# Performance work log

Measured on AMD Instinct MI355X. Metric: run time of the kernel, lower is better.

## Reference

```python
import jax, jax.numpy as jnp
import numpy as np

B, S, H = 2, 2048, 2048
FFN = 1024
E = 8
TOP_K = 2


def setup_inputs() -> dict:
    key = jax.random.key(0)
    ks = jax.random.split(key, 5)
    scale = 0.02
    hidden_states = jax.random.normal(ks[0], (B, S, H), dtype=jnp.float32)
    Wg = jax.random.normal(ks[1], (E, H), dtype=jnp.float32) * scale   # gate: Linear(H, E) weight
    W1 = jax.random.normal(ks[2], (E, FFN, H), dtype=jnp.float32) * scale  # stacked w1 per expert
    W3 = jax.random.normal(ks[3], (E, FFN, H), dtype=jnp.float32) * scale  # stacked w3 per expert
    W2 = jax.random.normal(ks[4], (E, H, FFN), dtype=jnp.float32) * scale  # stacked w2 per expert
    bias = jnp.zeros((E,), dtype=jnp.float32)  # e_score_correction_bias buffer
    return {"hidden_states": hidden_states, "Wg": Wg, "W1": W1, "W2": W2, "W3": W3, "bias": bias}


def reference(hidden_states, Wg, W1, W2, W3, bias):
    bsz, seq_len, hidden_dim = hidden_states.shape
    x = hidden_states.reshape(-1, hidden_dim)                 # [T, H]
    router_logits = x @ Wg.T                                  # [T, E]
    routing_weights = jax.nn.sigmoid(router_logits.astype(jnp.float32))
    scores = routing_weights + bias                           # bias only affects selection
    _, top_k_index = jax.lax.top_k(scores, TOP_K)             # [T, K]
    top_k_weights = jnp.take_along_axis(routing_weights, top_k_index, axis=1)
    top_k_weights = top_k_weights / top_k_weights.sum(axis=-1, keepdims=True)
    top_k_weights = top_k_weights.astype(x.dtype)
    # per-token per-expert combine weight (0 for non-selected experts)
    one_hot = jax.nn.one_hot(top_k_index, Wg.shape[0], dtype=x.dtype)  # [T, K, E]
    expert_w = jnp.einsum('tk,tke->te', top_k_weights, one_hot)        # [T, E]
    # SwiGLU expert MLPs applied via stacked (grouped) GEMMs
    h1 = jnp.einsum('th,efh->tef', x, W1)                     # [T, E, FFN]
    h3 = jnp.einsum('th,efh->tef', x, W3)
    g = jax.nn.silu(h1) * h3 * expert_w[:, :, None]           # scale before down-proj
    out = jnp.einsum('tef,ehf->th', g, W2)                    # weighted combine
    return out.reshape(bsz, seq_len, hidden_dim)
```

## Files before the change

kernel.cpp:

```cpp
#include <hip/hip_runtime.h>
#include <hip/hip_bf16.h>


#define T_TOK 4096
#define H_DIM 2048
#define FFN_D 1024
#define NE    8

typedef __attribute__((ext_vector_type(8))) short          bf16x8;
typedef __attribute__((ext_vector_type(4))) float          f32x4;
typedef __attribute__((ext_vector_type(4))) unsigned short us4;

__device__ __forceinline__ unsigned short f2bf(float f) {
  unsigned u = __builtin_bit_cast(unsigned, f);
  u += 0x7fffu + ((u >> 16) & 1u);
  return (unsigned short)(u >> 16);
}
__device__ __forceinline__ float bf2f(unsigned short u) {
  return __builtin_bit_cast(float, ((unsigned)u) << 16);
}
__device__ __forceinline__ void async16(const void* g, void* l) {
  __builtin_amdgcn_global_load_lds((const __attribute__((address_space(1))) void*)g,
                                   (__attribute__((address_space(3))) void*)l, 16, 0, 0);
}

__global__ void router2_kernel(const float* __restrict__ x,
                               const float* __restrict__ Wg,
                               const float* __restrict__ bias,
                               unsigned* __restrict__ epair,
                               float* __restrict__ wpair,
                               unsigned short* __restrict__ Xb) {
  const int wv   = threadIdx.x >> 6;
  const int lane = threadIdx.x & 63;
  const int t    = blockIdx.x * 4 + wv;

  const float4* xr = (const float4*)(x + (size_t)t * H_DIM);
  us4*          xb = (us4*)(Xb + (size_t)t * H_DIM);

  float acc[NE];
#pragma unroll
  for (int e = 0; e < NE; e++) acc[e] = 0.f;

#pragma unroll
  for (int j = 0; j < 8; j++) {
    int i4 = j * 64 + lane;
    float4 v = xr[i4];
    us4 d; d.x = f2bf(v.x); d.y = f2bf(v.y); d.z = f2bf(v.z); d.w = f2bf(v.w);
    xb[i4] = d;
#pragma unroll
    for (int e = 0; e < NE; e++) {
      float4 w = ((const float4*)(Wg + e * H_DIM))[i4];
      acc[e] += v.x * w.x + v.y * w.y + v.z * w.z + v.w * w.w;
    }
  }
#pragma unroll
  for (int e = 0; e < NE; e++) {
#pragma unroll
    for (int m = 32; m >= 1; m >>= 1) acc[e] += __shfl_xor(acc[e], m, 64);
  }

  if (lane == 0) {
    float sig[NE], sc[NE];
#pragma unroll
    for (int e = 0; e < NE; e++) {
      sig[e] = 1.f / (1.f + expf(-acc[e]));
      sc[e]  = sig[e] + bias[e];
    }
    int i1 = 0; float v1 = sc[0];
#pragma unroll
    for (int e = 1; e < NE; e++) if (sc[e] > v1) { v1 = sc[e]; i1 = e; }
    int i2 = -1; float v2 = -1e30f;
#pragma unroll
    for (int e = 0; e < NE; e++) if (e != i1 && sc[e] > v2) { v2 = sc[e]; i2 = e; }
    float w1 = sig[i1], w2 = sig[i2];
    float s = w1 + w2;
    epair[t] = (unsigned)i1 | ((unsigned)i2 << 8);
    wpair[2 * t]     = w1 / s;
    wpair[2 * t + 1] = w2 / s;
  }
}

__global__ void compact_kernel(const unsigned* __restrict__ epair,
                               const float* __restrict__ wpair,
                               int* __restrict__ cnt,
                               int* __restrict__ base,
                               int* __restrict__ rows,
                               float* __restrict__ wts,
                               int* __restrict__ t2s) {
  const int e    = threadIdx.x >> 6;
  const int lane = threadIdx.x & 63;
  const unsigned long long ltmask = ((unsigned long long)1 << lane) - 1;
  __shared__ int cnts[NE];

  int count = 0;
  for (int c = 0; c < T_TOK; c += 64) {
    int t = c + lane;
    unsigned ep = epair[t];
    bool m1 = ((ep & 255u) == (unsigned)e);
    bool m2 = (((ep >> 8) & 255u) == (unsigned)e);
    unsigned long long b1 = __ballot(m1);
    if (m1) {
      int p = count + __popcll(b1 & ltmask);
      rows[e * T_TOK + p] = t;
      wts [e * T_TOK + p] = wpair[2 * t];
      t2s[2 * t] = (e << 12) | p;
    }
    count += __popcll(b1);
    unsigned long long b2 = __ballot(m2);
    if (m2) {
      int p = count + __popcll(b2 & ltmask);
      rows[e * T_TOK + p] = t;
      wts [e * T_TOK + p] = wpair[2 * t + 1];
      t2s[2 * t + 1] = (e << 12) | p;
    }
    count += __popcll(b2);
  }
  if (lane == 0) { cnts[e] = count; cnt[e] = count; }
  __syncthreads();
  if (threadIdx.x == 0) {
    int s = 0;
    for (int i = 0; i < NE; i++) { base[i] = s; s += cnts[i]; }
    base[NE] = s;
  }
}

__global__ void convert2_kernel(const float* __restrict__ a, unsigned short* __restrict__ da,
                                const float* __restrict__ b, unsigned short* __restrict__ db) {
  const size_t N4 = (size_t)NE * FFN_D * H_DIM / 4;
  size_t i = (size_t)blockIdx.x * 256 + threadIdx.x;
  const float* s; unsigned short* d;
  if (i < N4) { s = a; d = da; } else { s = b; d = db; i -= N4; }
  float4 v = ((const float4*)s)[i];
  us4 o; o.x = f2bf(v.x); o.y = f2bf(v.y); o.z = f2bf(v.z); o.w = f2bf(v.w);
  ((us4*)d)[i] = o;
}
__global__ void convert_kernel(const float* __restrict__ s, unsigned short* __restrict__ d) {
  size_t i = (size_t)blockIdx.x * 256 + threadIdx.x;
  float4 v = ((const float4*)s)[i];
  us4 o; o.x = f2bf(v.x); o.y = f2bf(v.y); o.z = f2bf(v.z); o.w = f2bf(v.w);
  ((us4*)d)[i] = o;
}

__launch_bounds__(256)
__global__ void upproj_fast(const unsigned short* __restrict__ Xb,
                            const unsigned short* __restrict__ W1b,
                            const unsigned short* __restrict__ W3b,
                            const int* __restrict__ cnt,
                            const int* __restrict__ base,
                            const int* __restrict__ rows,
                            const float* __restrict__ wts,
                            unsigned short* __restrict__ G) {
  const int e  = blockIdx.z;
  const int m0 = blockIdx.y * 128;
  const int n0 = blockIdx.x * 64;
  const int ce = cnt[e];
  if (m0 >= ce) return;

  __shared__ __align__(16) unsigned short As [2 * 128 * 32];
  __shared__ __align__(16) unsigned short B1s[2 * 64 * 32];
  __shared__ __align__(16) unsigned short B3s[2 * 64 * 32];
  __shared__ int   t_ids[128];
  __shared__ float w_lds[128];

  const int tid = threadIdx.x;
  if (tid < 128) {
    int i = m0 + tid;
    if (i < ce) { t_ids[tid] = rows[e * T_TOK + i]; w_lds[tid] = wts[e * T_TOK + i]; }
    else        { t_ids[tid] = 0;                   w_lds[tid] = 0.f; }
  }
  __syncthreads();

  const int lane = tid & 63;
  const int wv   = tid >> 6;

  const unsigned short* gA[2];
#pragma unroll
  for (int c = 0; c < 2; c++) {
    int r = wv * 32 + c * 16 + (lane >> 2);
    gA[c] = Xb + (size_t)t_ids[r] * H_DIM + (lane & 3) * 8;
  }
  const size_t wrow = (size_t)(n0 + wv * 16 + (lane >> 2));
  const unsigned short* gB1 = W1b + (size_t)e * FFN_D * H_DIM + wrow * H_DIM + (lane & 3) * 8;
  const unsigned short* gB3 = W3b + (size_t)e * FFN_D * H_DIM + wrow * H_DIM + (lane & 3) * 8;

  const int wm = (wv & 1) * 64;
  const int wn = (wv >> 1) * 32;
  const int qk = (lane >> 4) * 8;
  const int lr = lane & 15;

  f32x4 acc1[4][2], acc3[4][2];
#pragma unroll
  for (int mi = 0; mi < 4; mi++)
#pragma unroll
    for (int ni = 0; ni < 2; ni++) { acc1[mi][ni] = (f32x4)0.f; acc3[mi][ni] = (f32x4)0.f; }

  for (int kt = 0; kt < H_DIM; kt += 64) {
#pragma unroll
    for (int h = 0; h < 2; h++) {
      async16(gA[0] + kt + h * 32, &As [h * 4096 + (wv * 32 + 0)  * 32]);
      async16(gA[1] + kt + h * 32, &As [h * 4096 + (wv * 32 + 16) * 32]);
      async16(gB1   + kt + h * 32, &B1s[h * 2048 + (wv * 16) * 32]);
      async16(gB3   + kt + h * 32, &B3s[h * 2048 + (wv * 16) * 32]);
    }
    __syncthreads();

#pragma unroll
    for (int h = 0; h < 2; h++) {
      bf16x8 a[4], b1[2], b3[2];
#pragma unroll
      for (int mi = 0; mi < 4; mi++)
        a[mi] = *(const bf16x8*)&As[h * 4096 + (wm + mi * 16 + lr) * 32 + qk];
#pragma unroll
      for (int ni = 0; ni < 2; ni++) {
        b1[ni] = *(const bf16x8*)&B1s[h * 2048 + (wn + ni * 16 + lr) * 32 + qk];
        b3[ni] = *(const bf16x8*)&B3s[h * 2048 + (wn + ni * 16 + lr) * 32 + qk];
      }
#pragma unroll
      for (int mi = 0; mi < 4; mi++)
#pragma unroll
        for (int ni = 0; ni < 2; ni++) {
          acc1[mi][ni] = __builtin_amdgcn_mfma_f32_16x16x32_bf16(a[mi], b1[ni], acc1[mi][ni], 0, 0, 0);
          acc3[mi][ni] = __builtin_amdgcn_mfma_f32_16x16x32_bf16(a[mi], b3[ni], acc3[mi][ni], 0, 0, 0);
        }
    }
    __syncthreads();
  }

  const int be = base[e];
#pragma unroll
  for (int mi = 0; mi < 4; mi++)
#pragma unroll
    for (int ni = 0; ni < 2; ni++)
#pragma unroll
      for (int r = 0; r < 4; r++) {
        int row = wm + mi * 16 + (lane >> 4) * 4 + r;
        int col = wn + ni * 16 + lr;
        int i = m0 + row;
        if (i < ce) {
          float h1 = acc1[mi][ni][r];
          float h3 = acc3[mi][ni][r];
          float g  = h1 / (1.f + expf(-h1)) * h3 * w_lds[row];
          G[(size_t)(be + i) * FFN_D + n0 + col] = f2bf(g);
        }
      }
}

__launch_bounds__(256)
__global__ void downproj_fast(const unsigned short* __restrict__ G,
                              const unsigned short* __restrict__ W2b,
                              const int* __restrict__ cnt,
                              const int* __restrict__ base,
                              unsigned short* __restrict__ Gd) {
  const int e  = blockIdx.z;
  const int m0 = blockIdx.y * 128;
  const int n0 = blockIdx.x * 128;
  const int ce = cnt[e];
  if (m0 >= ce) return;
  const int be = base[e];

  __shared__ __align__(16) unsigned short As[2 * 128 * 32];
  __shared__ __align__(16) unsigned short Bs[2 * 128 * 32];

  const int tid  = threadIdx.x;
  const int lane = tid & 63;
  const int wv   = tid >> 6;

  const unsigned short* gA[2];
  const unsigned short* gB[2];
#pragma unroll
  for (int c = 0; c < 2; c++) {
    int r = m0 + wv * 32 + c * 16 + (lane >> 2);
    if (r >= ce) r = ce - 1;
    gA[c] = G + (size_t)(be + r) * FFN_D + (lane & 3) * 8;
    int rb = wv * 32 + c * 16 + (lane >> 2);
    gB[c] = W2b + (size_t)e * H_DIM * FFN_D + (size_t)(n0 + rb) * FFN_D + (lane & 3) * 8;
  }

  const int wm = (wv & 1) * 64;
  const int wn = (wv >> 1) * 64;
  const int qk = (lane >> 4) * 8;
  const int lr = lane & 15;

  f32x4 acc[4][4];
#pragma unroll
  for (int mi = 0; mi < 4; mi++)
#pragma unroll
    for (int ni = 0; ni < 4; ni++) acc[mi][ni] = (f32x4)0.f;

  for (int kt = 0; kt < FFN_D; kt += 64) {
#pragma unroll
    for (int h = 0; h < 2; h++) {
      async16(gA[0] + kt + h * 32, &As[h * 4096 + (wv * 32 + 0)  * 32]);
      async16(gA[1] + kt + h * 32, &As[h * 4096 + (wv * 32 + 16) * 32]);
      async16(gB[0] + kt + h * 32, &Bs[h * 4096 + (wv * 32 + 0)  * 32]);
      async16(gB[1] + kt + h * 32, &Bs[h * 4096 + (wv * 32 + 16) * 32]);
    }
    __syncthreads();

#pragma unroll
    for (int h = 0; h < 2; h++) {
      bf16x8 a[4], b[4];
#pragma unroll
      for (int mi = 0; mi < 4; mi++)
        a[mi] = *(const bf16x8*)&As[h * 4096 + (wm + mi * 16 + lr) * 32 + qk];
#pragma unroll
      for (int ni = 0; ni < 4; ni++)
        b[ni] = *(const bf16x8*)&Bs[h * 4096 + (wn + ni * 16 + lr) * 32 + qk];
#pragma unroll
      for (int mi = 0; mi < 4; mi++)
#pragma unroll
        for (int ni = 0; ni < 4; ni++)
          acc[mi][ni] = __builtin_amdgcn_mfma_f32_16x16x32_bf16(a[mi], b[ni], acc[mi][ni], 0, 0, 0);
    }
    __syncthreads();
  }

#pragma unroll
  for (int mi = 0; mi < 4; mi++)
#pragma unroll
    for (int ni = 0; ni < 4; ni++)
#pragma unroll
      for (int r = 0; r < 4; r++) {
        int row = wm + mi * 16 + (lane >> 4) * 4 + r;
        int col = wn + ni * 16 + lr;
        int i = m0 + row;
        if (i < ce)
          Gd[(size_t)(be + i) * H_DIM + n0 + col] = f2bf(acc[mi][ni][r]);
      }
}

__global__ void combine_kernel(const unsigned short* __restrict__ Gd,
                               const int* __restrict__ base,
                               const int* __restrict__ tok2slot,
                               float* __restrict__ out) {
  const int t = blockIdx.x;
  const int v1 = tok2slot[2 * t], v2 = tok2slot[2 * t + 1];
  const int s1 = base[v1 >> 12] + (v1 & 4095);
  const int s2 = base[v2 >> 12] + (v2 & 4095);
  const us4* r1 = (const us4*)(Gd + (size_t)s1 * H_DIM);
  const us4* r2 = (const us4*)(Gd + (size_t)s2 * H_DIM);
  float4* o = (float4*)(out + (size_t)t * H_DIM);
#pragma unroll
  for (int j = 0; j < 2; j++) {
    int i = j * 256 + threadIdx.x;
    us4 a = r1[i], b = r2[i];
    float4 r;
    r.x = bf2f(a.x) + bf2f(b.x);
    r.y = bf2f(a.y) + bf2f(b.y);
    r.z = bf2f(a.z) + bf2f(b.z);
    r.w = bf2f(a.w) + bf2f(b.w);
    o[i] = r;
  }
}

extern "C" void kernel_launch(void* const* d_in, const int* in_sizes, int n_in,
                              void* d_out, int out_size, void* d_ws, size_t ws_size,
                              hipStream_t stream) {
  (void)in_sizes; (void)n_in; (void)out_size; (void)ws_size;
  const float* x    = (const float*)d_in[0];
  const float* Wg   = (const float*)d_in[1];
  const float* W1   = (const float*)d_in[2];
  const float* W2   = (const float*)d_in[3];
  const float* W3   = (const float*)d_in[4];
  const float* bias = (const float*)d_in[5];
  float* out = (float*)d_out;

  char* ws = (char*)d_ws;
  const size_t OFF_CNT   = 0;
  const size_t OFF_BASE  = 64;
  const size_t OFF_T2S   = 1024;
  const size_t OFF_ROWS  = 65536;
  const size_t OFF_WTS   = OFF_ROWS + 131072;
  const size_t OFF_EPAIR = OFF_WTS + 131072;
  const size_t OFF_WPAIR = OFF_EPAIR + 16384;
  const size_t OFF_XB    = 1048576;
  const size_t OFF_W1B   = OFF_XB + 16777216;
  const size_t OFF_W3B   = OFF_W1B + 33554432;
  const size_t OFF_G     = OFF_W3B + 33554432;

  int*   cnt   = (int*)(ws + OFF_CNT);
  int*   base  = (int*)(ws + OFF_BASE);
  int*   t2s   = (int*)(ws + OFF_T2S);
  int*   rows  = (int*)(ws + OFF_ROWS);
  float* wts   = (float*)(ws + OFF_WTS);
  unsigned* epair = (unsigned*)(ws + OFF_EPAIR);
  float* wpair = (float*)(ws + OFF_WPAIR);
  unsigned short* Xb  = (unsigned short*)(ws + OFF_XB);
  unsigned short* W1b = (unsigned short*)(ws + OFF_W1B);
  unsigned short* W3b = (unsigned short*)(ws + OFF_W3B);
  unsigned short* W2b = (unsigned short*)(ws + OFF_W3B);
  unsigned short* Gd  = (unsigned short*)(ws + OFF_W1B);
  unsigned short* G   = (unsigned short*)(ws + OFF_G);

  router2_kernel<<<T_TOK / 4, 256, 0, stream>>>(x, Wg, bias, epair, wpair, Xb);
  compact_kernel<<<1, 512, 0, stream>>>(epair, wpair, cnt, base, rows, wts, t2s);

  const size_t N4 = (size_t)NE * FFN_D * H_DIM / 4;
  convert2_kernel<<<(unsigned)(2 * N4 / 256), 256, 0, stream>>>(W1, W1b, W3, W3b);

  dim3 g2(FFN_D / 64, T_TOK / 128, NE);
  upproj_fast<<<g2, 256, 0, stream>>>(Xb, W1b, W3b, cnt, base, rows, wts, G);

  convert_kernel<<<(unsigned)(N4 / 256), 256, 0, stream>>>(W2, W2b);

  dim3 g3(H_DIM / 128, T_TOK / 128, NE);
  downproj_fast<<<g3, 256, 0, stream>>>(G, W2b, cnt, base, Gd);

  combine_kernel<<<T_TOK, 256, 0, stream>>>(Gd, base, t2s, out);
}
```

Baseline: 465.9 us.

## Merge weight conversions and token compaction into one kernel; shrink GEMM K-step

Folds the compact kernel and all three fp32-to-bf16 weight conversions into a single launch. The last block does the compaction, so that serial single-block step overlaps with the bandwidth-bound conversion. W2b gets its own workspace region, no longer aliasing W3b, so all conversions can happen before the up-projection. Both GEMM kernels change their K loop from 64 to 32 per iteration, halving LDS footprint. This may raise occupancy but doubles the number of barriers.

```diff
diff --git a/kernel.cpp b/kernel.cpp
--- a/kernel.cpp
+++ b/kernel.cpp
@@ -80,13 +80,28 @@
   }
 }
 
-__global__ void compact_kernel(const unsigned* __restrict__ epair,
-                               const float* __restrict__ wpair,
-                               int* __restrict__ cnt,
-                               int* __restrict__ base,
-                               int* __restrict__ rows,
-                               float* __restrict__ wts,
-                               int* __restrict__ t2s) {
+#define N4_PER_W ((size_t)NE * FFN_D * H_DIM / 4)
+#define NB_CONV  ((unsigned)(3 * N4_PER_W / 512))
+
+__global__ void convert_all_kernel(const float* __restrict__ W1, unsigned short* __restrict__ W1b,
+                                   const float* __restrict__ W3, unsigned short* __restrict__ W3b,
+                                   const float* __restrict__ W2, unsigned short* __restrict__ W2b,
+                                   const unsigned* __restrict__ epair,
+                                   const float* __restrict__ wpair,
+                                   int* __restrict__ cnt, int* __restrict__ base,
+                                   int* __restrict__ rows, float* __restrict__ wts,
+                                   int* __restrict__ t2s) {
+  if (blockIdx.x < NB_CONV) {
+    size_t i = (size_t)blockIdx.x * 512 + threadIdx.x;
+    const float* s; unsigned short* d;
+    if (i < N4_PER_W)            { s = W1; d = W1b; }
+    else if (i < 2 * N4_PER_W)   { s = W3; d = W3b; i -= N4_PER_W; }
+    else                         { s = W2; d = W2b; i -= 2 * N4_PER_W; }
+    float4 v = ((const float4*)s)[i];
+    us4 o; o.x = f2bf(v.x); o.y = f2bf(v.y); o.z = f2bf(v.z); o.w = f2bf(v.w);
+    ((us4*)d)[i] = o;
+    return;
+  }
   const int e    = threadIdx.x >> 6;
   const int lane = threadIdx.x & 63;
   const unsigned long long ltmask = ((unsigned long long)1 << lane) - 1;
@@ -124,23 +139,6 @@
   }
 }
 
-__global__ void convert2_kernel(const float* __restrict__ a, unsigned short* __restrict__ da,
-                                const float* __restrict__ b, unsigned short* __restrict__ db) {
-  const size_t N4 = (size_t)NE * FFN_D * H_DIM / 4;
-  size_t i = (size_t)blockIdx.x * 256 + threadIdx.x;
-  const float* s; unsigned short* d;
-  if (i < N4) { s = a; d = da; } else { s = b; d = db; i -= N4; }
-  float4 v = ((const float4*)s)[i];
-  us4 o; o.x = f2bf(v.x); o.y = f2bf(v.y); o.z = f2bf(v.z); o.w = f2bf(v.w);
-  ((us4*)d)[i] = o;
-}
-__global__ void convert_kernel(const float* __restrict__ s, unsigned short* __restrict__ d) {
-  size_t i = (size_t)blockIdx.x * 256 + threadIdx.x;
-  float4 v = ((const float4*)s)[i];
-  us4 o; o.x = f2bf(v.x); o.y = f2bf(v.y); o.z = f2bf(v.z); o.w = f2bf(v.w);
-  ((us4*)d)[i] = o;
-}
-
 __launch_bounds__(256)
 __global__ void upproj_fast(const unsigned short* __restrict__ Xb,
                             const unsigned short* __restrict__ W1b,
@@ -156,9 +154,9 @@
   const int ce = cnt[e];
   if (m0 >= ce) return;
 
-  __shared__ __align__(16) unsigned short As [2 * 128 * 32];
-  __shared__ __align__(16) unsigned short B1s[2 * 64 * 32];
-  __shared__ __align__(16) unsigned short B3s[2 * 64 * 32];
+  __shared__ __align__(16) unsigned short As [128 * 32];
+  __shared__ __align__(16) unsigned short B1s[64 * 32];
+  __shared__ __align__(16) unsigned short B3s[64 * 32];
   __shared__ int   t_ids[128];
   __shared__ float w_lds[128];
 
@@ -182,6 +180,10 @@
   const size_t wrow = (size_t)(n0 + wv * 16 + (lane >> 2));
   const unsigned short* gB1 = W1b + (size_t)e * FFN_D * H_DIM + wrow * H_DIM + (lane & 3) * 8;
   const unsigned short* gB3 = W3b + (size_t)e * FFN_D * H_DIM + wrow * H_DIM + (lane & 3) * 8;
+  unsigned short* lA0 = &As [(wv * 32 + 0)  * 32];
+  unsigned short* lA1 = &As [(wv * 32 + 16) * 32];
+  unsigned short* lB1 = &B1s[(wv * 16) * 32];
+  unsigned short* lB3 = &B3s[(wv * 16) * 32];
 
   const int wm = (wv & 1) * 64;
   const int wn = (wv >> 1) * 32;
@@ -194,35 +196,29 @@
 #pragma unroll
     for (int ni = 0; ni < 2; ni++) { acc1[mi][ni] = (f32x4)0.f; acc3[mi][ni] = (f32x4)0.f; }
 
-  for (int kt = 0; kt < H_DIM; kt += 64) {
-#pragma unroll
-    for (int h = 0; h < 2; h++) {
-      async16(gA[0] + kt + h * 32, &As [h * 4096 + (wv * 32 + 0)  * 32]);
-      async16(gA[1] + kt + h * 32, &As [h * 4096 + (wv * 32 + 16) * 32]);
-      async16(gB1   + kt + h * 32, &B1s[h * 2048 + (wv * 16) * 32]);
-      async16(gB3   + kt + h * 32, &B3s[h * 2048 + (wv * 16) * 32]);
+  for (int kt = 0; kt < H_DIM; kt += 32) {
+    async16(gA[0] + kt, lA0);
+    async16(gA[1] + kt, lA1);
+    async16(gB1 + kt,   lB1);
+    async16(gB3 + kt,   lB3);
+    __syncthreads();
+
+    bf16x8 a[4], b1[2], b3[2];
+#pragma unroll
+    for (int mi = 0; mi < 4; mi++)
+      a[mi] = *(const bf16x8*)&As[(wm + mi * 16 + lr) * 32 + qk];
+#pragma unroll
+    for (int ni = 0; ni < 2; ni++) {
+      b1[ni] = *(const bf16x8*)&B1s[(wn + ni * 16 + lr) * 32 + qk];
+      b3[ni] = *(const bf16x8*)&B3s[(wn + ni * 16 + lr) * 32 + qk];
     }
-    __syncthreads();
-
-#pragma unroll
-    for (int h = 0; h < 2; h++) {
-      bf16x8 a[4], b1[2], b3[2];
-#pragma unroll
-      for (int mi = 0; mi < 4; mi++)
-        a[mi] = *(const bf16x8*)&As[h * 4096 + (wm + mi * 16 + lr) * 32 + qk];
+#pragma unroll
+    for (int mi = 0; mi < 4; mi++)
 #pragma unroll
       for (int ni = 0; ni < 2; ni++) {
-        b1[ni] = *(const bf16x8*)&B1s[h * 2048 + (wn + ni * 16 + lr) * 32 + qk];
-        b3[ni] = *(const bf16x8*)&B3s[h * 2048 + (wn + ni * 16 + lr) * 32 + qk];
+        acc1[mi][ni] = __builtin_amdgcn_mfma_f32_16x16x32_bf16(a[mi], b1[ni], acc1[mi][ni], 0, 0, 0);
+        acc3[mi][ni] = __builtin_amdgcn_mfma_f32_16x16x32_bf16(a[mi], b3[ni], acc3[mi][ni], 0, 0, 0);
       }
-#pragma unroll
-      for (int mi = 0; mi < 4; mi++)
-#pragma unroll
-        for (int ni = 0; ni < 2; ni++) {
-          acc1[mi][ni] = __builtin_amdgcn_mfma_f32_16x16x32_bf16(a[mi], b1[ni], acc1[mi][ni], 0, 0, 0);
-          acc3[mi][ni] = __builtin_amdgcn_mfma_f32_16x16x32_bf16(a[mi], b3[ni], acc3[mi][ni], 0, 0, 0);
-        }
-    }
     __syncthreads();
   }
 
@@ -258,8 +254,8 @@
   if (m0 >= ce) return;
   const int be = base[e];
 
-  __shared__ __align__(16) unsigned short As[2 * 128 * 32];
-  __shared__ __align__(16) unsigned short Bs[2 * 128 * 32];
+  __shared__ __align__(16) unsigned short As[128 * 32];
+  __shared__ __align__(16) unsigned short Bs[128 * 32];
 
   const int tid  = threadIdx.x;
   const int lane = tid & 63;
@@ -275,6 +271,8 @@
     int rb = wv * 32 + c * 16 + (lane >> 2);
     gB[c] = W2b + (size_t)e * H_DIM * FFN_D + (size_t)(n0 + rb) * FFN_D + (lane & 3) * 8;
   }
+  unsigned short* lA[2] = { &As[(wv * 32 + 0) * 32], &As[(wv * 32 + 16) * 32] };
+  unsigned short* lB[2] = { &Bs[(wv * 32 + 0) * 32], &Bs[(wv * 32 + 16) * 32] };
 
   const int wm = (wv & 1) * 64;
   const int wn = (wv >> 1) * 64;
@@ -287,31 +285,25 @@
 #pragma unroll
     for (int ni = 0; ni < 4; ni++) acc[mi][ni] = (f32x4)0.f;
 
-  for (int kt = 0; kt < FFN_D; kt += 64) {
-#pragma unroll
-    for (int h = 0; h < 2; h++) {
-      async16(gA[0] + kt + h * 32, &As[h * 4096 + (wv * 32 + 0)  * 32]);
-      async16(gA[1] + kt + h * 32, &As[h * 4096 + (wv * 32 + 16) * 32]);
-      async16(gB[0] + kt + h * 32, &Bs[h * 4096 + (wv * 32 + 0)  * 32]);
-      async16(gB[1] + kt + h * 32, &Bs[h * 4096 + (wv * 32 + 16) * 32]);
-    }
+  for (int kt = 0; kt < FFN_D; kt += 32) {
+    async16(gA[0] + kt, lA[0]);
+    async16(gA[1] + kt, lA[1]);
+    async16(gB[0] + kt, lB[0]);
+    async16(gB[1] + kt, lB[1]);
     __syncthreads();
 
-#pragma unroll
-    for (int h = 0; h < 2; h++) {
-      bf16x8 a[4], b[4];
-#pragma unroll
-      for (int mi = 0; mi < 4; mi++)
-        a[mi] = *(const bf16x8*)&As[h * 4096 + (wm + mi * 16 + lr) * 32 + qk];
+    bf16x8 a[4], b[4];
+#pragma unroll
+    for (int mi = 0; mi < 4; mi++)
+      a[mi] = *(const bf16x8*)&As[(wm + mi * 16 + lr) * 32 + qk];
+#pragma unroll
+    for (int ni = 0; ni < 4; ni++)
+      b[ni] = *(const bf16x8*)&Bs[(wn + ni * 16 + lr) * 32 + qk];
+#pragma unroll
+    for (int mi = 0; mi < 4; mi++)
 #pragma unroll
       for (int ni = 0; ni < 4; ni++)
-        b[ni] = *(const bf16x8*)&Bs[h * 4096 + (wn + ni * 16 + lr) * 32 + qk];
-#pragma unroll
-      for (int mi = 0; mi < 4; mi++)
-#pragma unroll
-        for (int ni = 0; ni < 4; ni++)
-          acc[mi][ni] = __builtin_amdgcn_mfma_f32_16x16x32_bf16(a[mi], b[ni], acc[mi][ni], 0, 0, 0);
-    }
+        acc[mi][ni] = __builtin_amdgcn_mfma_f32_16x16x32_bf16(a[mi], b[ni], acc[mi][ni], 0, 0, 0);
     __syncthreads();
   }
 
@@ -377,6 +369,7 @@
   const size_t OFF_W1B   = OFF_XB + 16777216;
   const size_t OFF_W3B   = OFF_W1B + 33554432;
   const size_t OFF_G     = OFF_W3B + 33554432;
+  const size_t OFF_W2B   = OFF_G + 16777216;
 
   int*   cnt   = (int*)(ws + OFF_CNT);
   int*   base  = (int*)(ws + OFF_BASE);
@@ -388,21 +381,18 @@
   unsigned short* Xb  = (unsigned short*)(ws + OFF_XB);
   unsigned short* W1b = (unsigned short*)(ws + OFF_W1B);
   unsigned short* W3b = (unsigned short*)(ws + OFF_W3B);
-  unsigned short* W2b = (unsigned short*)(ws + OFF_W3B);
+  unsigned short* W2b = (unsigned short*)(ws + OFF_W2B);
   unsigned short* Gd  = (unsigned short*)(ws + OFF_W1B);
   unsigned short* G   = (unsigned short*)(ws + OFF_G);
 
   router2_kernel<<<T_TOK / 4, 256, 0, stream>>>(x, Wg, bias, epair, wpair, Xb);
-  compact_kernel<<<1, 512, 0, stream>>>(epair, wpair, cnt, base, rows, wts, t2s);
-
-  const size_t N4 = (size_t)NE * FFN_D * H_DIM / 4;
-  convert2_kernel<<<(unsigned)(2 * N4 / 256), 256, 0, stream>>>(W1, W1b, W3, W3b);
+
+  convert_all_kernel<<<NB_CONV + 1, 512, 0, stream>>>(W1, W1b, W3, W3b, W2, W2b,
+                                                      epair, wpair, cnt, base, rows, wts, t2s);
 
   dim3 g2(FFN_D / 64, T_TOK / 128, NE);
   upproj_fast<<<g2, 256, 0, stream>>>(Xb, W1b, W3b, cnt, base, rows, wts, G);
 
-  convert_kernel<<<(unsigned)(N4 / 256), 256, 0, stream>>>(W2, W2b);
-
   dim3 g3(H_DIM / 128, T_TOK / 128, NE);
   downproj_fast<<<g3, 256, 0, stream>>>(G, W2b, cnt, base, Gd);
 
```

Measured after the change: 461.5 us. No clear change (-1.0%).
